# Kernel tuning notes

Measured on AMD Instinct MI355X. Metric: run time of the kernel, lower is better.

Reference implementation:

```python
import jax, jax.numpy as jnp
import numpy as np

N_NODES = 50000
N_EDGES = 262144
HID = 256
N_CLS = 2


def setup_inputs() -> dict:
    key = jax.random.key(0)
    ks = jax.random.split(key, 6)
    node_repr = jax.random.normal(ks[0], (N_NODES, HID), dtype=jnp.float32)
    src = jax.random.randint(ks[1], (N_EDGES,), 0, N_NODES, dtype=jnp.int64)
    dst = jax.random.randint(ks[2], (N_EDGES,), 0, N_NODES, dtype=jnp.int64)
    # Linear weights stored as (in, out); init ~ torch default scale
    W1 = jax.random.normal(ks[3], (4 * HID, 2 * HID), dtype=jnp.float32) * (1.0 / np.sqrt(4 * HID))
    b1 = jnp.zeros((2 * HID,), dtype=jnp.float32)
    W2 = jax.random.normal(ks[4], (2 * HID, N_CLS), dtype=jnp.float32) * (1.0 / np.sqrt(2 * HID))
    b2 = jnp.zeros((N_CLS,), dtype=jnp.float32)
    return {"node_repr": node_repr, "src": src, "dst": dst,
            "W1": W1, "b1": b1, "W2": W2, "b2": b2}


def reference(node_repr, src, dst, W1, b1, W2, b2):
    h_i = node_repr[src]                      # [E, H] gather
    h_j = node_repr[dst]                      # [E, H] gather
    edge_input = jnp.concatenate(
        [h_i, h_j, jnp.abs(h_i - h_j), h_i * h_j], axis=1)  # [E, 4H]
    h = jax.nn.relu(edge_input @ W1 + b1)     # [E, 2H]; dropout = identity (eval)
    return h @ W2 + b2                        # [E, C]
```

## Files before the change

### kernel.cpp

```cpp
#include <hip/hip_runtime.h>

#define N_NODES 50000
#define E_EDGES 262144

typedef __attribute__((ext_vector_type(8))) short bf16x8;
typedef __attribute__((ext_vector_type(4))) float f32x4;

union V16 { uint4 u; bf16x8 h; };

__device__ __forceinline__ unsigned rne_pack(float a, float b) {
  unsigned ua = __float_as_uint(a); ua += 0x7fffu + ((ua >> 16) & 1u);
  unsigned ub = __float_as_uint(b); ub += 0x7fffu + ((ub >> 16) & 1u);
  return (ua >> 16) | (ub & 0xffff0000u);
}
__device__ __forceinline__ float bflo(unsigned u) { return __uint_as_float(u << 16); }
__device__ __forceinline__ float bfhi(unsigned u) { return __uint_as_float(u & 0xffff0000u); }
__device__ __forceinline__ unsigned perm_pack(float a, float b) {
  return __builtin_amdgcn_perm(__float_as_uint(b), __float_as_uint(a), 0x07060302u);
}
__device__ __forceinline__ void async_gather16(const void* gptr, void* lptr) {
  __builtin_amdgcn_global_load_lds(
      (const __attribute__((address_space(1))) void*)gptr,
      (__attribute__((address_space(3))) void*)lptr, 16, 0, 0);
}

__global__ void cvt_node_kernel(const float* __restrict__ x, unsigned short* __restrict__ y) {
  int i = (blockIdx.x * 256 + threadIdx.x) * 8;
  float4 f0 = *(const float4*)(x + i);
  float4 f1 = *(const float4*)(x + i + 4);
  uint4 o;
  o.x = rne_pack(f0.x, f0.y);
  o.y = rne_pack(f0.z, f0.w);
  o.z = rne_pack(f1.x, f1.y);
  o.w = rne_pack(f1.z, f1.w);
  *(uint4*)(y + i) = o;
}

__global__ void prep_w1pp2_kernel(const float* __restrict__ w1, unsigned short* __restrict__ w1pp2) {
  int t = blockIdx.x * 256 + threadIdx.x;
  int step = t >> 13;
  int rem = t & 8191;
  int sq = rem >> 9;
  int col = rem & 511;
  int s = sq >> 2, qd = sq & 3;
  int k0 = s * 256 + step * 32 + qd * 8;
  float f[8];
#pragma unroll
  for (int i = 0; i < 8; ++i) f[i] = w1[(size_t)(k0 + i) * 512 + col];
  uint4 o;
  o.x = rne_pack(f[0], f[1]);
  o.y = rne_pack(f[2], f[3]);
  o.z = rne_pack(f[4], f[5]);
  o.w = rne_pack(f[6], f[7]);
  *(uint4*)(w1pp2 + (size_t)t * 8) = o;
}

__global__ void init_out_kernel(float* __restrict__ out, const float* __restrict__ b2) {
  int i = blockIdx.x * 256 + threadIdx.x;
  float2 v; v.x = b2[0]; v.y = b2[1];
  *(float2*)(out + (size_t)i * 2) = v;
}

__global__ __launch_bounds__(256, 2) void edge_mlp_kernel(
    const unsigned short* __restrict__ nodeb,
    const unsigned short* __restrict__ w1pp2,
    const int* __restrict__ src,
    const int* __restrict__ dst,
    const float* __restrict__ b1,
    const float* __restrict__ w2,
    float* __restrict__ out) {
  __shared__ char smem[32768];

  const int tid = threadIdx.x;
  const int wid = tid >> 6;
  const int lane = tid & 63;
  const int quad = lane >> 4;
  const int l16 = lane & 15;
  const int bx = blockIdx.x;
  const int m_idx = ((bx >> 5) << 3) + (bx & 7);
  const int n_idx = (bx >> 3) & 3;
  const int wave_m = wid >> 1;
  const int wave_n = wid & 1;
  const int row0 = m_idx * 128;
  const int wrow0 = row0 + wave_m * 64;
  const int n0 = n_idx * 128 + wave_n * 64;

  const char* nodeB = (const char*)nodeb;
  const char* w1B = (const char*)w1pp2;

  const int eh = tid >> 2;
  const unsigned qsw = (unsigned)(((tid & 3) ^ ((tid >> 3) & 3)) << 4);
  const unsigned oi0 = ((unsigned)src[row0 + eh] << 9) + qsw;
  const unsigned oi1 = ((unsigned)src[row0 + 64 + eh] << 9) + qsw;
  const unsigned oj0 = ((unsigned)dst[row0 + eh] << 9) + qsw;
  const unsigned oj1 = ((unsigned)dst[row0 + 64 + eh] << 9) + qsw;
  const unsigned sdst = (unsigned)(wid * 1024);

  unsigned bOff[4];
#pragma unroll
  for (int s = 0; s < 4; ++s)
    bOff[s] = (unsigned)((s * 4 + quad) * 8192 + (n0 + l16) * 16);

  const unsigned aR = (unsigned)((wave_m * 64 + l16) * 64 + ((quad ^ ((l16 >> 1) & 3)) << 4));

  f32x4 acc[4][4];
#pragma unroll
  for (int mt = 0; mt < 4; ++mt)
#pragma unroll
    for (int nt = 0; nt < 4; ++nt)
      acc[mt][nt] = (f32x4){0.f, 0.f, 0.f, 0.f};

  async_gather16(nodeB + oi0, smem + sdst);
  async_gather16(nodeB + oi1, smem + 4096 + sdst);
  async_gather16(nodeB + oj0, smem + 8192 + sdst);
  async_gather16(nodeB + oj1, smem + 12288 + sdst);
  __syncthreads();

  int p = 0;
#pragma unroll 1
  for (int step = 0; step < 8; ++step) {
    const char* Acur = smem + (p << 14);
    if (step < 7) {
      const unsigned aoN = (unsigned)(step + 1) * 64u;
      char* Aalt = smem + ((p ^ 1) << 14);
      async_gather16(nodeB + (oi0 + aoN), Aalt + sdst);
      async_gather16(nodeB + (oi1 + aoN), Aalt + 4096 + sdst);
      async_gather16(nodeB + (oj0 + aoN), Aalt + 8192 + sdst);
      async_gather16(nodeB + (oj1 + aoN), Aalt + 12288 + sdst);
    }
    const unsigned wstep = (unsigned)step * 131072u;
    V16 bf[4][4];
#pragma unroll
    for (int s = 0; s < 4; ++s)
#pragma unroll
      for (int nt = 0; nt < 4; ++nt)
        bf[s][nt].u = *(const uint4*)(w1B + (wstep + bOff[s]) + nt * 256);
    V16 hi[4], hj[4];
#pragma unroll
    for (int mt = 0; mt < 4; ++mt) {
      hi[mt].u = *(const uint4*)(Acur + aR + mt * 1024);
      hj[mt].u = *(const uint4*)(Acur + 8192 + aR + mt * 1024);
    }
#pragma unroll
    for (int sl = 0; sl < 2; ++sl) {
#pragma unroll
      for (int mt = 0; mt < 4; ++mt) {
        bf16x8 af = (sl == 0) ? hi[mt].h : hj[mt].h;
#pragma unroll
        for (int nt = 0; nt < 4; ++nt)
          acc[mt][nt] = __builtin_amdgcn_mfma_f32_16x16x32_bf16(af, bf[sl][nt].h, acc[mt][nt], 0, 0, 0);
      }
    }
#pragma unroll
    for (int mt = 0; mt < 4; ++mt) {
      const unsigned hw[4] = {hi[mt].u.x, hi[mt].u.y, hi[mt].u.z, hi[mt].u.w};
      const unsigned jw[4] = {hj[mt].u.x, hj[mt].u.y, hj[mt].u.z, hj[mt].u.w};
      unsigned d[4], pr[4];
#pragma unroll
      for (int w = 0; w < 4; ++w) {
        float i0 = bflo(hw[w]), i1 = bfhi(hw[w]);
        float j0 = bflo(jw[w]), j1 = bfhi(jw[w]);
        d[w] = perm_pack(i0 - j0, i1 - j1) & 0x7fff7fffu;
        pr[w] = perm_pack(i0 * j0, i1 * j1);
      }
      V16 a2, a3;
      a2.u = make_uint4(d[0], d[1], d[2], d[3]);
      a3.u = make_uint4(pr[0], pr[1], pr[2], pr[3]);
#pragma unroll
      for (int nt = 0; nt < 4; ++nt)
        acc[mt][nt] = __builtin_amdgcn_mfma_f32_16x16x32_bf16(a2.h, bf[2][nt].h, acc[mt][nt], 0, 0, 0);
#pragma unroll
      for (int nt = 0; nt < 4; ++nt)
        acc[mt][nt] = __builtin_amdgcn_mfma_f32_16x16x32_bf16(a3.h, bf[3][nt].h, acc[mt][nt], 0, 0, 0);
    }
    __syncthreads();
    p ^= 1;
  }

#pragma unroll
  for (int mt = 0; mt < 4; ++mt) {
    float pc0[4] = {0.f, 0.f, 0.f, 0.f};
    float pc1[4] = {0.f, 0.f, 0.f, 0.f};
#pragma unroll
    for (int nt = 0; nt < 4; ++nt) {
      int gc = n0 + nt * 16 + l16;
      float b1v = b1[gc];
      float w20 = w2[gc * 2 + 0];
      float w21 = w2[gc * 2 + 1];
#pragma unroll
      for (int r = 0; r < 4; ++r) {
        float v = fmaxf(acc[mt][nt][r] + b1v, 0.f);
        pc0[r] = fmaf(v, w20, pc0[r]);
        pc1[r] = fmaf(v, w21, pc1[r]);
      }
    }
#pragma unroll
    for (int r = 0; r < 4; ++r) {
      float s0 = pc0[r], s1 = pc1[r];
#pragma unroll
      for (int off = 1; off < 16; off <<= 1) {
        s0 += __shfl_xor(s0, off);
        s1 += __shfl_xor(s1, off);
      }
      int e = wrow0 + mt * 16 + quad * 4 + r;
      if (l16 == 0) unsafeAtomicAdd(&out[(size_t)e * 2 + 0], s0);
      if (l16 == 1) unsafeAtomicAdd(&out[(size_t)e * 2 + 1], s1);
    }
  }
}

extern "C" void kernel_launch(void* const* d_in, const int* in_sizes, int n_in,
                              void* d_out, int out_size, void* d_ws, size_t ws_size,
                              hipStream_t stream) {
  const float* node = (const float*)d_in[0];
  const int* src = (const int*)d_in[1];
  const int* dst = (const int*)d_in[2];
  const float* W1 = (const float*)d_in[3];
  const float* b1 = (const float*)d_in[4];
  const float* W2 = (const float*)d_in[5];
  const float* b2 = (const float*)d_in[6];
  float* out = (float*)d_out;

  unsigned short* nodeb = (unsigned short*)d_ws;
  unsigned short* w1pp2 = (unsigned short*)((char*)d_ws + 25600000);

  cvt_node_kernel<<<6250, 256, 0, stream>>>(node, nodeb);
  prep_w1pp2_kernel<<<256, 256, 0, stream>>>(W1, w1pp2);
  init_out_kernel<<<1024, 256, 0, stream>>>(out, b2);
  edge_mlp_kernel<<<8192, 256, 0, stream>>>(nodeb, w1pp2, src, dst, b1, W2, out);
}
```

Baseline: 472.9 us.

## Retile edge MLP to 256-edge x 64-column blocks with doubled LDS buffers

Changes the block tile from 128 edges x 128 hidden columns (2x2 waves) to 256 edges x 64 columns, with each wave owning 64 edges across the full 64 columns. Each block now gathers 256 edge pairs per step into a 64 KB double-buffered LDS area, and the W1 fragment loads are issued before the async gathers. This cuts weight fragment reloads per wave but doubles node-gather traffic per column tile (8 column tiles instead of 4), and the larger LDS footprint may limit occupancy.

```diff
diff --git a/kernel.cpp b/kernel.cpp
--- a/kernel.cpp
+++ b/kernel.cpp
@@ -69,7 +69,7 @@
     const float* __restrict__ b1,
     const float* __restrict__ w2,
     float* __restrict__ out) {
-  __shared__ char smem[32768];
+  __shared__ char smem[65536];
 
   const int tid = threadIdx.x;
   const int wid = tid >> 6;
@@ -77,31 +77,32 @@
   const int quad = lane >> 4;
   const int l16 = lane & 15;
   const int bx = blockIdx.x;
-  const int m_idx = ((bx >> 5) << 3) + (bx & 7);
-  const int n_idx = (bx >> 3) & 3;
-  const int wave_m = wid >> 1;
-  const int wave_n = wid & 1;
-  const int row0 = m_idx * 128;
-  const int wrow0 = row0 + wave_m * 64;
-  const int n0 = n_idx * 128 + wave_n * 64;
+  const int xc = bx & 7;
+  const int t2 = bx >> 3;
+  const int n_idx = t2 & 7;
+  const int m_idx = (t2 >> 3) * 8 + xc;
+  const int row0 = m_idx * 256;
+  const int wrow0 = row0 + wid * 64;
+  const int n0 = n_idx * 64;
 
   const char* nodeB = (const char*)nodeb;
   const char* w1B = (const char*)w1pp2;
 
-  const int eh = tid >> 2;
-  const unsigned qsw = (unsigned)(((tid & 3) ^ ((tid >> 3) & 3)) << 4);
-  const unsigned oi0 = ((unsigned)src[row0 + eh] << 9) + qsw;
-  const unsigned oi1 = ((unsigned)src[row0 + 64 + eh] << 9) + qsw;
-  const unsigned oj0 = ((unsigned)dst[row0 + eh] << 9) + qsw;
-  const unsigned oj1 = ((unsigned)dst[row0 + 64 + eh] << 9) + qsw;
-  const unsigned sdst = (unsigned)(wid * 1024);
-
+  unsigned oi[4], oj[4];
+#pragma unroll
+  for (int c = 0; c < 4; ++c) {
+    int e = (wid * 4 + c) * 16 + (lane >> 2);
+    unsigned qg = (unsigned)(((lane & 3) ^ ((lane >> 3) & 3)) << 4);
+    oi[c] = ((unsigned)src[row0 + e] << 9) + qg;
+    oj[c] = ((unsigned)dst[row0 + e] << 9) + qg;
+  }
   unsigned bOff[4];
 #pragma unroll
   for (int s = 0; s < 4; ++s)
     bOff[s] = (unsigned)((s * 4 + quad) * 8192 + (n0 + l16) * 16);
-
-  const unsigned aR = (unsigned)((wave_m * 64 + l16) * 64 + ((quad ^ ((l16 >> 1) & 3)) << 4));
+  const char* w1s = w1B;
+
+  const unsigned aR = (unsigned)((wid * 64 + l16) * 64 + ((quad ^ ((l16 >> 1) & 3)) << 4));
 
   f32x4 acc[4][4];
 #pragma unroll
@@ -110,36 +111,37 @@
     for (int nt = 0; nt < 4; ++nt)
       acc[mt][nt] = (f32x4){0.f, 0.f, 0.f, 0.f};
 
-  async_gather16(nodeB + oi0, smem + sdst);
-  async_gather16(nodeB + oi1, smem + 4096 + sdst);
-  async_gather16(nodeB + oj0, smem + 8192 + sdst);
-  async_gather16(nodeB + oj1, smem + 12288 + sdst);
+#pragma unroll
+  for (int c = 0; c < 4; ++c) {
+    async_gather16(nodeB + oi[c], smem + (wid * 4 + c) * 1024);
+    async_gather16(nodeB + oj[c], smem + 16384 + (wid * 4 + c) * 1024);
+  }
   __syncthreads();
 
   int p = 0;
 #pragma unroll 1
   for (int step = 0; step < 8; ++step) {
-    const char* Acur = smem + (p << 14);
+    const char* Acur = smem + (p << 15);
+    V16 bf[4][4];
+#pragma unroll
+    for (int s = 0; s < 4; ++s)
+#pragma unroll
+      for (int nt = 0; nt < 4; ++nt)
+        bf[s][nt].u = *(const uint4*)(w1s + bOff[s] + nt * 256);
     if (step < 7) {
       const unsigned aoN = (unsigned)(step + 1) * 64u;
-      char* Aalt = smem + ((p ^ 1) << 14);
-      async_gather16(nodeB + (oi0 + aoN), Aalt + sdst);
-      async_gather16(nodeB + (oi1 + aoN), Aalt + 4096 + sdst);
-      async_gather16(nodeB + (oj0 + aoN), Aalt + 8192 + sdst);
-      async_gather16(nodeB + (oj1 + aoN), Aalt + 12288 + sdst);
-    }
-    const unsigned wstep = (unsigned)step * 131072u;
-    V16 bf[4][4];
-#pragma unroll
-    for (int s = 0; s < 4; ++s)
-#pragma unroll
-      for (int nt = 0; nt < 4; ++nt)
-        bf[s][nt].u = *(const uint4*)(w1B + (wstep + bOff[s]) + nt * 256);
+      char* Aalt = smem + ((p ^ 1) << 15);
+#pragma unroll
+      for (int c = 0; c < 4; ++c) {
+        async_gather16(nodeB + (oi[c] + aoN), Aalt + (wid * 4 + c) * 1024);
+        async_gather16(nodeB + (oj[c] + aoN), Aalt + 16384 + (wid * 4 + c) * 1024);
+      }
+    }
     V16 hi[4], hj[4];
 #pragma unroll
     for (int mt = 0; mt < 4; ++mt) {
       hi[mt].u = *(const uint4*)(Acur + aR + mt * 1024);
-      hj[mt].u = *(const uint4*)(Acur + 8192 + aR + mt * 1024);
+      hj[mt].u = *(const uint4*)(Acur + 16384 + aR + mt * 1024);
     }
 #pragma unroll
     for (int sl = 0; sl < 2; ++sl) {
@@ -174,6 +176,7 @@
         acc[mt][nt] = __builtin_amdgcn_mfma_f32_16x16x32_bf16(a3.h, bf[3][nt].h, acc[mt][nt], 0, 0, 0);
     }
     __syncthreads();
+    w1s += 131072;
     p ^= 1;
   }
 
```

Result: slower. 493.6 us (+4.4%).
